# Optimization experiments

Measured on AMD Instinct MI355X. Metric: run time of the kernel, lower is better.

## Reference

```python
import jax, jax.numpy as jnp
import numpy as np

N = 100000          # nodes
E = 1600000         # edges (avg degree 16)
DIN = 64
DOUT = 64
EXPERTS = 3
GATE_C = 4
TEMP = 101.0        # batch=0 < decay_lim: 100 - 0 + final_temperature(1.0)


def setup_inputs() -> dict:
    key = jax.random.key(0)
    ks = jax.random.split(key, 6)
    x = jax.random.normal(ks[0], (N, DIN), dtype=jnp.float32)
    edge_index = jax.random.randint(ks[1], (2, E), 0, N, dtype=jnp.int32)
    gate_features = jax.random.normal(ks[2], (N, GATE_C), dtype=jnp.float32)
    # per-expert GCN linear weights/bias (PyG GCNConv: lin then bias)
    W = jax.random.normal(ks[3], (EXPERTS, DIN, DOUT), dtype=jnp.float32) / np.sqrt(DIN).astype(np.float32)
    b = jnp.zeros((EXPERTS, DOUT), dtype=jnp.float32)
    # gating nn.Linear(gate_channels, experts, bias=False); stored as [GATE_C, EXPERTS] so y = gf @ Wg
    Wg = jax.random.normal(ks[4], (GATE_C, EXPERTS), dtype=jnp.float32) / np.sqrt(GATE_C).astype(np.float32)
    return {"x": x, "edge_index": edge_index, "gate_features": gate_features,
            "W": W, "b": b, "Wg": Wg}


def reference(x, edge_index, gate_features, W, b, Wg):
    n = x.shape[0]
    # --- GCN normalization with self-loops (PyG GCNConv defaults) ---
    loops = jnp.arange(n, dtype=edge_index.dtype)
    rows = jnp.concatenate([edge_index[0], loops])   # source nodes, [E+N]
    cols = jnp.concatenate([edge_index[1], loops])   # target nodes, [E+N]
    deg = jax.ops.segment_sum(jnp.ones(rows.shape, dtype=x.dtype), cols, num_segments=n)
    dinv = jnp.where(deg > 0, jax.lax.rsqrt(deg), 0.0)
    norm = dinv[rows] * dinv[cols]                   # [E+N]

    # --- gating network (softmax with decayed temperature) ---
    gate = jax.nn.softmax((gate_features @ Wg) / jnp.asarray(TEMP, x.dtype), axis=-1)  # [N, EXPERTS]

    # --- experts: GCN conv -> ReLU -> gate-weighted accumulation ---
    out = jnp.zeros((n, W.shape[-1]), dtype=x.dtype)
    for i in range(W.shape[0]):                      # small fixed expert count
        xw = x @ W[i]                                # [N, DOUT]
        msg = xw[rows] * norm[:, None]               # gather + scale, [E+N, DOUT]
        agg = jax.ops.segment_sum(msg, cols, num_segments=n) + b[i]
        out = out + gate[:, i:i + 1] * jax.nn.relu(agg)
    return out
```

## Files before the change

kernel.cpp:

```cpp
#include <hip/hip_runtime.h>
#include <hip/hip_bf16.h>

#define NN 100000
#define NE 1600000
#define NT 6250

#define NBUCK  511
#define BRANGE 196
#define CAPB   3584
#define CHUNK  4096
#define NCH    391

typedef __attribute__((ext_vector_type(8))) short bf16x8;
typedef __attribute__((ext_vector_type(4))) float f32x4;

__device__ inline float2 bf16x2_unpack(unsigned v) {
    float2 r;
    r.x = __uint_as_float(v << 16);
    r.y = __uint_as_float(v & 0xffff0000u);
    return r;
}
__device__ inline unsigned bf16x2_pack(float a, float b) {
    __hip_bfloat162 h2(__float2bfloat16(a), __float2bfloat16(b));
    unsigned u;
    __builtin_memcpy(&u, &h2, 4);
    return u;
}

__global__ __launch_bounds__(256) void bin_kernel(const int* __restrict__ rows,
                                                  const int* __restrict__ cols,
                                                  int* __restrict__ cur,
                                                  unsigned* __restrict__ eb) {
    __shared__ int hist[512];
    __shared__ int excl[512];
    __shared__ int lcur[512];
    __shared__ int gbase[512];
    __shared__ int s2[256];
    __shared__ unsigned staged[CHUNK];
    __shared__ unsigned short bktarr[CHUNK];
    int t = threadIdx.x;
    int base = blockIdx.x * CHUNK;
    int cnt = min(CHUNK, NE - base);

    hist[t] = 0; hist[t + 256] = 0;
    __syncthreads();
    #pragma unroll
    for (int k = 0; k < CHUNK / 256; k++) {
        int i = k * 256 + t;
        if (i < cnt) {
            int c = cols[base + i];
            atomicAdd(&hist[(unsigned)c / BRANGE], 1);
        }
    }
    __syncthreads();
    int a0 = hist[2 * t], a1 = hist[2 * t + 1];
    s2[t] = a0 + a1;
    __syncthreads();
    #pragma unroll
    for (int off = 1; off < 256; off <<= 1) {
        int v = (t >= off) ? s2[t - off] : 0;
        __syncthreads();
        s2[t] += v;
        __syncthreads();
    }
    int pe = (t > 0) ? s2[t - 1] : 0;
    excl[2 * t] = pe;      excl[2 * t + 1] = pe + a0;
    lcur[2 * t] = pe;      lcur[2 * t + 1] = pe + a0;
    gbase[2 * t]     = a0 ? atomicAdd(cur + 2 * t, a0) : 0;
    gbase[2 * t + 1] = a1 ? atomicAdd(cur + 2 * t + 1, a1) : 0;
    __syncthreads();
    #pragma unroll
    for (int k = 0; k < CHUNK / 256; k++) {
        int i = k * 256 + t;
        if (i < cnt) {
            int c = cols[base + i];
            int r = rows[base + i];
            int bkt = (unsigned)c / BRANGE;
            int lp = atomicAdd(&lcur[bkt], 1);
            staged[lp] = ((unsigned)(c - bkt * BRANGE) << 24) | (unsigned)r;
            bktarr[lp] = (unsigned short)bkt;
        }
    }
    __syncthreads();
    #pragma unroll
    for (int k = 0; k < CHUNK / 256; k++) {
        int i = k * 256 + t;
        if (i < cnt) {
            int bkt = bktarr[i];
            int pos = gbase[bkt] + (i - excl[bkt]);
            if (pos < CAPB) eb[(size_t)bkt * CAPB + pos] = staged[i];
        }
    }
}

__global__ __launch_bounds__(256) void nodesort_kernel(const int* __restrict__ cur,
                                                       const unsigned* __restrict__ eb,
                                                       int* __restrict__ srcs2,
                                                       int2* __restrict__ nsd) {
    __shared__ int hist[256];
    __shared__ int sx[256];
    __shared__ int lcur[BRANGE];
    int b = blockIdx.x, t = threadIdx.x;
    hist[t] = 0;
    __syncthreads();
    int cnt = min(cur[b], CAPB);
    const unsigned* seg = eb + (size_t)b * CAPB;
    for (int e = t; e < cnt; e += 256) atomicAdd(&hist[seg[e] >> 24], 1);
    __syncthreads();
    int h = hist[t];
    sx[t] = h;
    __syncthreads();
    #pragma unroll
    for (int off = 1; off < 256; off <<= 1) {
        int v = (t >= off) ? sx[t - off] : 0;
        __syncthreads();
        sx[t] += v;
        __syncthreads();
    }
    int ex = (t > 0) ? sx[t - 1] : 0;
    if (t < BRANGE) {
        lcur[t] = ex;
        int n = b * BRANGE + t;
        if (n < NN) nsd[n] = make_int2(ex, h);
    }
    __syncthreads();
    for (int e = t; e < cnt; e += 256) {
        unsigned rec = seg[e];
        int p = atomicAdd(&lcur[rec >> 24], 1);
        srcs2[(size_t)b * CAPB + p] = rec & 0xFFFFFFu;
    }
}

__global__ __launch_bounds__(256) void xscale_kernel(const float* __restrict__ x,
                                                     const int2* __restrict__ nsd,
                                                     unsigned* __restrict__ xs) {
    int i = blockIdx.x * 256 + threadIdx.x;
    int n = i >> 5;
    int d = (i & 31) * 2;
    float2 v = *(const float2*)(x + (size_t)n * 64 + d);
    float dv = rsqrtf((float)(nsd[n].y + 1));
    xs[i] = bf16x2_pack(v.x * dv, v.y * dv);
}

__global__ __launch_bounds__(256) void gather_kernel(const int* __restrict__ srcs2,
                                                     const int2* __restrict__ nsd,
                                                     const unsigned* __restrict__ xs,
                                                     unsigned* __restrict__ hbu) {
    int wave = threadIdx.x >> 6;
    int n = blockIdx.x * 4 + wave;
    int lane = threadIdx.x & 63;
    int sub = lane >> 5;
    int dp = lane & 31;

    int2 sd = nsd[n];
    int deg = sd.y;
    int bkt = (unsigned)n / BRANGE;
    const int* seg = srcs2 + (size_t)bkt * CAPB + sd.x;

    float2 acc = make_float2(0.f, 0.f);
    int e = sub;
    for (; e + 14 < deg; e += 16) {
        int r0 = seg[e];      int r1 = seg[e + 2];
        int r2 = seg[e + 4];  int r3 = seg[e + 6];
        int r4 = seg[e + 8];  int r5 = seg[e + 10];
        int r6 = seg[e + 12]; int r7 = seg[e + 14];
        float2 v0 = bf16x2_unpack(xs[(size_t)r0 * 32 + dp]);
        float2 v1 = bf16x2_unpack(xs[(size_t)r1 * 32 + dp]);
        float2 v2 = bf16x2_unpack(xs[(size_t)r2 * 32 + dp]);
        float2 v3 = bf16x2_unpack(xs[(size_t)r3 * 32 + dp]);
        float2 v4 = bf16x2_unpack(xs[(size_t)r4 * 32 + dp]);
        float2 v5 = bf16x2_unpack(xs[(size_t)r5 * 32 + dp]);
        float2 v6 = bf16x2_unpack(xs[(size_t)r6 * 32 + dp]);
        float2 v7 = bf16x2_unpack(xs[(size_t)r7 * 32 + dp]);
        acc.x += ((v0.x + v1.x) + (v2.x + v3.x)) + ((v4.x + v5.x) + (v6.x + v7.x));
        acc.y += ((v0.y + v1.y) + (v2.y + v3.y)) + ((v4.y + v5.y) + (v6.y + v7.y));
    }
    for (; e + 6 < deg; e += 8) {
        int r0 = seg[e];     int r1 = seg[e + 2];
        int r2 = seg[e + 4]; int r3 = seg[e + 6];
        float2 v0 = bf16x2_unpack(xs[(size_t)r0 * 32 + dp]);
        float2 v1 = bf16x2_unpack(xs[(size_t)r1 * 32 + dp]);
        float2 v2 = bf16x2_unpack(xs[(size_t)r2 * 32 + dp]);
        float2 v3 = bf16x2_unpack(xs[(size_t)r3 * 32 + dp]);
        acc.x += (v0.x + v1.x) + (v2.x + v3.x);
        acc.y += (v0.y + v1.y) + (v2.y + v3.y);
    }
    for (; e + 2 < deg; e += 4) {
        int r0 = seg[e]; int r1 = seg[e + 2];
        float2 v0 = bf16x2_unpack(xs[(size_t)r0 * 32 + dp]);
        float2 v1 = bf16x2_unpack(xs[(size_t)r1 * 32 + dp]);
        acc.x += v0.x + v1.x;
        acc.y += v0.y + v1.y;
    }
    for (; e < deg; e += 2) {
        float2 v = bf16x2_unpack(xs[(size_t)seg[e] * 32 + dp]);
        acc.x += v.x;
        acc.y += v.y;
    }
    acc.x += __shfl_xor(acc.x, 32);
    acc.y += __shfl_xor(acc.y, 32);
    float2 sv = bf16x2_unpack(xs[(size_t)n * 32 + dp]);
    float dn = rsqrtf((float)(deg + 1));
    unsigned packed = bf16x2_pack((acc.x + sv.x) * dn, (acc.y + sv.y) * dn);
    if (sub == 0) hbu[(size_t)n * 32 + dp] = packed;
}

__global__ void wpack_kernel(const float* __restrict__ W, __hip_bfloat16* __restrict__ Bp) {
    int idx = blockIdx.x * 256 + threadIdx.x;
    if (idx >= 12288) return;
    int j    = idx & 7;
    int lane = (idx >> 3) & 63;
    int rest = idx >> 9;
    int t    = rest % 12;
    int kh   = rest / 12;
    int k    = kh * 32 + (lane >> 4) * 8 + j;
    int col  = t * 16 + (lane & 15);
    int i    = col >> 6;
    int d    = col & 63;
    Bp[idx] = __float2bfloat16(W[(i * 64 + k) * 64 + d]);
}

__global__ __launch_bounds__(256) void mfma_kernel(const __hip_bfloat16* __restrict__ hb,
                                                   const short* __restrict__ Bp,
                                                   const float* __restrict__ b,
                                                   const float* __restrict__ gf,
                                                   const float* __restrict__ Wg,
                                                   float* __restrict__ out) {
    int wave = threadIdx.x >> 6;
    int lane = threadIdx.x & 63;
    int tile = blockIdx.x * 4 + wave;
    if (tile >= NT) return;
    int n0 = tile * 16;
    int m = lane & 15, quad = lane >> 4;

    const short* hrow = (const short*)hb + ((size_t)(n0 + m)) * 64 + quad * 8;
    bf16x8 a0 = *(const bf16x8*)(hrow);
    bf16x8 a1 = *(const bf16x8*)(hrow + 32);

    f32x4 acc[12];
    #pragma unroll
    for (int t = 0; t < 12; t++) acc[t] = (f32x4)(0.0f);

    #pragma unroll
    for (int kh = 0; kh < 2; kh++) {
        bf16x8 a = kh ? a1 : a0;
        #pragma unroll
        for (int t = 0; t < 12; t++) {
            bf16x8 bf = *(const bf16x8*)(Bp + ((size_t)((kh * 12 + t) * 64 + lane)) * 8);
            acc[t] = __builtin_amdgcn_mfma_f32_16x16x32_bf16(a, bf, acc[t], 0, 0, 0);
        }
    }

    float wg[12];
    #pragma unroll
    for (int k = 0; k < 12; k++) wg[k] = Wg[k];

    #pragma unroll
    for (int reg = 0; reg < 4; reg++) {
        int n = n0 + quad * 4 + reg;
        float4 g = ((const float4*)gf)[n];
        float l0 = (g.x*wg[0] + g.y*wg[3] + g.z*wg[6] + g.w*wg[9])  * (1.0f/101.0f);
        float l1 = (g.x*wg[1] + g.y*wg[4] + g.z*wg[7] + g.w*wg[10]) * (1.0f/101.0f);
        float l2 = (g.x*wg[2] + g.y*wg[5] + g.z*wg[8] + g.w*wg[11]) * (1.0f/101.0f);
        float mx = fmaxf(l0, fmaxf(l1, l2));
        float e0 = __expf(l0 - mx), e1 = __expf(l1 - mx), e2 = __expf(l2 - mx);
        float inv = 1.0f / (e0 + e1 + e2);
        float g0 = e0 * inv, g1 = e1 * inv, g2 = e2 * inv;
        #pragma unroll
        for (int dpos = 0; dpos < 4; dpos++) {
            int d = dpos * 16 + m;
            float v0 = acc[0*4 + dpos][reg] + b[0*64 + d];
            float v1 = acc[1*4 + dpos][reg] + b[1*64 + d];
            float v2 = acc[2*4 + dpos][reg] + b[2*64 + d];
            float o = g0 * fmaxf(v0, 0.f) + g1 * fmaxf(v1, 0.f) + g2 * fmaxf(v2, 0.f);
            out[(size_t)n * 64 + d] = o;
        }
    }
}

extern "C" void kernel_launch(void* const* d_in, const int* in_sizes, int n_in,
                              void* d_out, int out_size, void* d_ws, size_t ws_size,
                              hipStream_t stream) {
    const float* x  = (const float*)d_in[0];
    const int*   ei = (const int*)d_in[1];
    const float* gf = (const float*)d_in[2];
    const float* W  = (const float*)d_in[3];
    const float* b  = (const float*)d_in[4];
    const float* Wg = (const float*)d_in[5];
    float* out = (float*)d_out;
    const int* rows = ei;
    const int* cols = ei + NE;

    char* ws = (char*)d_ws;
    size_t off = 0;
    auto alloc = [&](size_t bytes) {
        char* p = ws + off;
        off = (off + bytes + 255) & ~(size_t)255;
        return p;
    };
    int*            cur    = (int*)alloc(512 * 4);
    unsigned*       eb     = (unsigned*)alloc((size_t)NBUCK * CAPB * 4);
    int*            srcs2  = (int*)alloc((size_t)NBUCK * CAPB * 4);
    int2*           nsd    = (int2*)alloc((size_t)NN * 8);
    unsigned*       xs     = (unsigned*)alloc((size_t)NN * 32 * 4);
    unsigned*       hbu    = (unsigned*)alloc((size_t)NN * 32 * 4);
    __hip_bfloat16* Bp     = (__hip_bfloat16*)alloc(12288 * 2);

    hipMemsetAsync(cur, 0, 512 * 4, stream);

    bin_kernel<<<NCH, 256, 0, stream>>>(rows, cols, cur, eb);
    nodesort_kernel<<<NBUCK, 256, 0, stream>>>(cur, eb, srcs2, nsd);
    xscale_kernel<<<NN * 32 / 256, 256, 0, stream>>>(x, nsd, xs);
    wpack_kernel<<<48, 256, 0, stream>>>(W, Bp);
    gather_kernel<<<NN / 4, 256, 0, stream>>>(srcs2, nsd, xs, hbu);
    mfma_kernel<<<(NT + 3) / 4, 256, 0, stream>>>((const __hip_bfloat16*)hbu,
                                                  (const short*)Bp, b, gf, Wg, out);
}
```

Baseline: 196.1 us.

## Gather one node per 16-lane group with 8-byte loads; widen sort and bin parallelism

The gather kernel now handles four nodes per wave, one per 16-lane group. Each group loads up to 16 neighbor indices with a single coalesced read, broadcasts them by shuffle, and each lane fetches 8 bytes (four bf16 features) per neighbor, with eight loads in flight. This replaces the old scheme of half-waves striding over neighbors followed by a cross-half reduction, and aims for more bytes per load and fewer idle lanes on low-degree nodes. The nodesort kernel now uses 512 threads per block and the bin kernel uses half-size chunks across twice as many blocks, to add parallelism in the preprocessing stages. Inactive tail slots still issue a redundant load of the first neighbor, and the smaller bin chunks add more global atomics on the bucket counters.

```diff
diff --git a/kernel.cpp b/kernel.cpp
--- a/kernel.cpp
+++ b/kernel.cpp
@@ -8,8 +8,8 @@
 #define NBUCK  511
 #define BRANGE 196
 #define CAPB   3584
-#define CHUNK  4096
-#define NCH    391
+#define CHUNK  2048
+#define NCH    782
 
 typedef __attribute__((ext_vector_type(8))) short bf16x8;
 typedef __attribute__((ext_vector_type(4))) float f32x4;
@@ -93,7 +93,7 @@
     }
 }
 
-__global__ __launch_bounds__(256) void nodesort_kernel(const int* __restrict__ cur,
+__global__ __launch_bounds__(512) void nodesort_kernel(const int* __restrict__ cur,
                                                        const unsigned* __restrict__ eb,
                                                        int* __restrict__ srcs2,
                                                        int2* __restrict__ nsd) {
@@ -101,30 +101,29 @@
     __shared__ int sx[256];
     __shared__ int lcur[BRANGE];
     int b = blockIdx.x, t = threadIdx.x;
-    hist[t] = 0;
+    if (t < 256) hist[t] = 0;
     __syncthreads();
     int cnt = min(cur[b], CAPB);
     const unsigned* seg = eb + (size_t)b * CAPB;
-    for (int e = t; e < cnt; e += 256) atomicAdd(&hist[seg[e] >> 24], 1);
-    __syncthreads();
-    int h = hist[t];
-    sx[t] = h;
+    for (int e = t; e < cnt; e += 512) atomicAdd(&hist[seg[e] >> 24], 1);
+    __syncthreads();
+    if (t < 256) sx[t] = hist[t];
     __syncthreads();
     #pragma unroll
     for (int off = 1; off < 256; off <<= 1) {
-        int v = (t >= off) ? sx[t - off] : 0;
+        int v = (t < 256 && t >= off) ? sx[t - off] : 0;
         __syncthreads();
-        sx[t] += v;
+        if (t < 256) sx[t] += v;
         __syncthreads();
     }
-    int ex = (t > 0) ? sx[t - 1] : 0;
     if (t < BRANGE) {
+        int ex = (t > 0) ? sx[t - 1] : 0;
         lcur[t] = ex;
         int n = b * BRANGE + t;
-        if (n < NN) nsd[n] = make_int2(ex, h);
-    }
-    __syncthreads();
-    for (int e = t; e < cnt; e += 256) {
+        if (n < NN) nsd[n] = make_int2(ex, hist[t]);
+    }
+    __syncthreads();
+    for (int e = t; e < cnt; e += 512) {
         unsigned rec = seg[e];
         int p = atomicAdd(&lcur[rec >> 24], 1);
         srcs2[(size_t)b * CAPB + p] = rec & 0xFFFFFFu;
@@ -146,63 +145,52 @@
                                                      const int2* __restrict__ nsd,
                                                      const unsigned* __restrict__ xs,
                                                      unsigned* __restrict__ hbu) {
+    int lane = threadIdx.x & 63;
     int wave = threadIdx.x >> 6;
-    int n = blockIdx.x * 4 + wave;
-    int lane = threadIdx.x & 63;
-    int sub = lane >> 5;
-    int dp = lane & 31;
-
+    int g  = lane >> 4;
+    int gl = lane & 15;
+    int gb = g << 4;
+
+    int n = blockIdx.x * 16 + wave * 4 + g;
     int2 sd = nsd[n];
     int deg = sd.y;
     int bkt = (unsigned)n / BRANGE;
     const int* seg = srcs2 + (size_t)bkt * CAPB + sd.x;
-
-    float2 acc = make_float2(0.f, 0.f);
-    int e = sub;
-    for (; e + 14 < deg; e += 16) {
-        int r0 = seg[e];      int r1 = seg[e + 2];
-        int r2 = seg[e + 4];  int r3 = seg[e + 6];
-        int r4 = seg[e + 8];  int r5 = seg[e + 10];
-        int r6 = seg[e + 12]; int r7 = seg[e + 14];
-        float2 v0 = bf16x2_unpack(xs[(size_t)r0 * 32 + dp]);
-        float2 v1 = bf16x2_unpack(xs[(size_t)r1 * 32 + dp]);
-        float2 v2 = bf16x2_unpack(xs[(size_t)r2 * 32 + dp]);
-        float2 v3 = bf16x2_unpack(xs[(size_t)r3 * 32 + dp]);
-        float2 v4 = bf16x2_unpack(xs[(size_t)r4 * 32 + dp]);
-        float2 v5 = bf16x2_unpack(xs[(size_t)r5 * 32 + dp]);
-        float2 v6 = bf16x2_unpack(xs[(size_t)r6 * 32 + dp]);
-        float2 v7 = bf16x2_unpack(xs[(size_t)r7 * 32 + dp]);
-        acc.x += ((v0.x + v1.x) + (v2.x + v3.x)) + ((v4.x + v5.x) + (v6.x + v7.x));
-        acc.y += ((v0.y + v1.y) + (v2.y + v3.y)) + ((v4.y + v5.y) + (v6.y + v7.y));
-    }
-    for (; e + 6 < deg; e += 8) {
-        int r0 = seg[e];     int r1 = seg[e + 2];
-        int r2 = seg[e + 4]; int r3 = seg[e + 6];
-        float2 v0 = bf16x2_unpack(xs[(size_t)r0 * 32 + dp]);
-        float2 v1 = bf16x2_unpack(xs[(size_t)r1 * 32 + dp]);
-        float2 v2 = bf16x2_unpack(xs[(size_t)r2 * 32 + dp]);
-        float2 v3 = bf16x2_unpack(xs[(size_t)r3 * 32 + dp]);
-        acc.x += (v0.x + v1.x) + (v2.x + v3.x);
-        acc.y += (v0.y + v1.y) + (v2.y + v3.y);
-    }
-    for (; e + 2 < deg; e += 4) {
-        int r0 = seg[e]; int r1 = seg[e + 2];
-        float2 v0 = bf16x2_unpack(xs[(size_t)r0 * 32 + dp]);
-        float2 v1 = bf16x2_unpack(xs[(size_t)r1 * 32 + dp]);
-        acc.x += v0.x + v1.x;
-        acc.y += v0.y + v1.y;
-    }
-    for (; e < deg; e += 2) {
-        float2 v = bf16x2_unpack(xs[(size_t)seg[e] * 32 + dp]);
-        acc.x += v.x;
-        acc.y += v.y;
-    }
-    acc.x += __shfl_xor(acc.x, 32);
-    acc.y += __shfl_xor(acc.y, 32);
-    float2 sv = bf16x2_unpack(xs[(size_t)n * 32 + dp]);
+    const uint2* xsv = (const uint2*)xs;
+
+    float4 acc = make_float4(0.f, 0.f, 0.f, 0.f);
+    for (int base = 0; base < deg; base += 16) {
+        int idx = 0;
+        if (base + gl < deg) idx = seg[base + gl];
+        int s0 = __shfl(idx, gb);
+        #pragma unroll
+        for (int c = 0; c < 16; c += 8) {
+            uint2 v[8];
+            #pragma unroll
+            for (int j = 0; j < 8; j++) {
+                int s = __shfl(idx, gb + c + j);
+                s = (base + c + j < deg) ? s : s0;
+                v[j] = xsv[(size_t)s * 16 + gl];
+            }
+            #pragma unroll
+            for (int j = 0; j < 8; j++) {
+                if (base + c + j < deg) {
+                    float2 f0 = bf16x2_unpack(v[j].x);
+                    float2 f1 = bf16x2_unpack(v[j].y);
+                    acc.x += f0.x; acc.y += f0.y;
+                    acc.z += f1.x; acc.w += f1.y;
+                }
+            }
+        }
+    }
+    uint2 svu = xsv[(size_t)n * 16 + gl];
+    float2 sv0 = bf16x2_unpack(svu.x);
+    float2 sv1 = bf16x2_unpack(svu.y);
     float dn = rsqrtf((float)(deg + 1));
-    unsigned packed = bf16x2_pack((acc.x + sv.x) * dn, (acc.y + sv.y) * dn);
-    if (sub == 0) hbu[(size_t)n * 32 + dp] = packed;
+    uint2 o;
+    o.x = bf16x2_pack((acc.x + sv0.x) * dn, (acc.y + sv0.y) * dn);
+    o.y = bf16x2_pack((acc.z + sv1.x) * dn, (acc.w + sv1.y) * dn);
+    ((uint2*)hbu)[(size_t)n * 16 + gl] = o;
 }
 
 __global__ void wpack_kernel(const float* __restrict__ W, __hip_bfloat16* __restrict__ Bp) {
@@ -309,10 +297,10 @@
     hipMemsetAsync(cur, 0, 512 * 4, stream);
 
     bin_kernel<<<NCH, 256, 0, stream>>>(rows, cols, cur, eb);
-    nodesort_kernel<<<NBUCK, 256, 0, stream>>>(cur, eb, srcs2, nsd);
+    nodesort_kernel<<<NBUCK, 512, 0, stream>>>(cur, eb, srcs2, nsd);
     xscale_kernel<<<NN * 32 / 256, 256, 0, stream>>>(x, nsd, xs);
     wpack_kernel<<<48, 256, 0, stream>>>(W, Bp);
-    gather_kernel<<<NN / 4, 256, 0, stream>>>(srcs2, nsd, xs, hbu);
+    gather_kernel<<<NN / 16, 256, 0, stream>>>(srcs2, nsd, xs, hbu);
     mfma_kernel<<<(NT + 3) / 4, 256, 0, stream>>>((const __hip_bfloat16*)hbu,
                                                   (const short*)Bp, b, gf, Wg, out);
 }
```

After: 194.7 us. Within noise of the previous version (-0.7%).
